# Kernel tuning notes

Hardware: AMD Instinct MI355X
Metric: run time of the kernel (lower is better)

## Reference

```python
import jax, jax.numpy as jnp
import numpy as np
import math

B, L, C_IN = 256, 128, 75
D_EMB = 128      # DataEmbedding d_model
D_MODEL = 126    # encoder d_model (= L-2 after ODConv valid conv k=3)
H = 6
D_HEAD = D_MODEL // H  # 21
D_FF = 2048
FACTOR = 5
K_NUM = 4        # ODConv kernel_num (default)
ATT_CH = 16      # max(int(128*0.0625), 16)
EPS = 1e-5


def _ln(x, g, b):
    m = x.mean(-1, keepdims=True)
    v = ((x - m) ** 2).mean(-1, keepdims=True)
    return (x - m) * jax.lax.rsqrt(v + EPS) * g + b


def _bn_eval(x, g, b):
    # eval-mode BatchNorm, running_mean=0 running_var=1
    return x * (g / np.sqrt(1.0 + EPS)) + b


def _conv1d(x, w, b=None):
    out = jax.lax.conv_general_dilated(x, w, (1,), 'VALID',
                                       dimension_numbers=('NCH', 'OIH', 'NCH'))
    if b is not None:
        out = out + b[None, :, None]
    return out


def _pos_embed(n, d):
    pos = np.arange(n)[:, None].astype(np.float32)
    div = np.exp(np.arange(0, d, 2).astype(np.float32) * (-math.log(10000.0) / d))
    pe = np.zeros((n, d), np.float32)
    pe[:, 0::2] = np.sin(pos * div)
    pe[:, 1::2] = np.cos(pos * div)
    return jnp.asarray(pe)


def _prob_attention(Q, K, V, key):
    # Informer ProbAttention, mask_flag=False. Q,K,V: [B,H,Lq,D]
    b, h, lq, d = Q.shape
    lk = K.shape[2]
    u_keys = min(FACTOR * int(np.ceil(np.log(lk))), lk)
    n_top = min(FACTOR * int(np.ceil(np.log(lq))), lq)
    idx = jax.random.randint(key, (lq, u_keys), 0, lk)     # sampled key ids per query
    K_s = K[:, :, idx, :]                                  # [B,H,Lq,u,D]
    qks = jnp.einsum('bhld,bhlud->bhlu', Q, K_s)
    M = qks.max(-1) - qks.sum(-1) / lk                     # sparsity measure
    _, top = jax.lax.top_k(M, n_top)                       # [B,H,n_top]
    Qr = jnp.take_along_axis(Q, top[..., None], axis=2)    # [B,H,n_top,D]
    scores = jnp.einsum('bhud,bhkd->bhuk', Qr, K) / np.sqrt(d).astype(np.float32)
    upd = jnp.einsum('bhuk,bhkd->bhud', jax.nn.softmax(scores, -1), V)
    ctx = jnp.broadcast_to(V.mean(2, keepdims=True), Q.shape)  # initial context
    bi = jnp.arange(b)[:, None, None]
    hi = jnp.arange(h)[None, :, None]
    return ctx.at[bi, hi, top].set(upd)


def _forward(x_enc, x_mark_enc, token_w, time_w, time_b,
             od_fc_w, od_bn_g, od_bn_b, od_ch_w, od_ch_b, od_fil_w, od_fil_b,
             od_sp_w, od_sp_b, od_ker_w, od_ker_b, od_weight,
             q_w, q_b, k_w, k_b, v_w, v_b, o_w, o_b,
             ffn1_w, ffn1_b, ffn2_w, ffn2_b, ln1_g, ln1_b, ln2_g, ln2_b,
             cl_w, cl_b, cl_bn_g, cl_bn_b, enc_ln_g, enc_ln_b, fc_w, fc_b):
    # ---- DataEmbedding (token circular conv + pos + timeF linear; dropout=eval) ----
    xt = jnp.pad(x_enc.transpose(0, 2, 1), ((0, 0), (0, 0), (1, 1)), mode='wrap')
    tok = _conv1d(xt, token_w).transpose(0, 2, 1)          # [B,L,128]
    emb = tok + _pos_embed(L, D_EMB)[None] + (x_mark_enc @ time_w + time_b)

    # ---- ODConv1d(128,128,k=3,pad=0) on [B,128,L] ----
    x = emb.transpose(0, 2, 1)                             # [B,128,L]
    gap = x.mean(-1)                                       # [B,128]
    a = jax.nn.relu(_bn_eval(gap @ od_fc_w, od_bn_g, od_bn_b))   # [B,16]
    ch_att = jax.nn.sigmoid(a @ od_ch_w + od_ch_b)         # [B,128]
    fil_att = jax.nn.sigmoid(a @ od_fil_w + od_fil_b)      # [B,128]
    sp_att = jax.nn.sigmoid(a @ od_sp_w + od_sp_b)         # [B,3]
    ker_att = jax.nn.softmax(a @ od_ker_w + od_ker_b, -1)  # [B,4]
    xc = x * ch_att[:, :, None]
    agg_w = jnp.einsum('bn,bj,noij->boij', ker_att, sp_att, od_weight)  # [B,128,128,3]
    lout = L - 2
    patches = jnp.stack([xc[:, :, j:j + lout] for j in range(3)], axis=2)  # [B,128,3,126]
    x = jnp.einsum('boij,bijt->bot', agg_w, patches) * fil_att[:, :, None]  # [B,128,126]
    # encoder reads this as (seq=128, d_model=126)

    key = jax.random.key(42)

    def enc_layer(xx, i):
        b, l, _ = xx.shape
        Q = (xx @ q_w[i] + q_b[i]).reshape(b, l, H, D_HEAD).transpose(0, 2, 1, 3)
        Kk = (xx @ k_w[i] + k_b[i]).reshape(b, l, H, D_HEAD).transpose(0, 2, 1, 3)
        Vv = (xx @ v_w[i] + v_b[i]).reshape(b, l, H, D_HEAD).transpose(0, 2, 1, 3)
        ctx = _prob_attention(Q, Kk, Vv, jax.random.fold_in(key, i))
        new_x = ctx.transpose(0, 2, 1, 3).reshape(b, l, D_MODEL) @ o_w[i] + o_b[i]
        xx = _ln(xx + new_x, ln1_g[i], ln1_b[i])
        y = jax.nn.gelu(xx @ ffn1_w[i] + ffn1_b[i], approximate=False)
        y = y @ ffn2_w[i] + ffn2_b[i]
        return _ln(xx + y, ln2_g[i], ln2_b[i])

    x = enc_layer(x, 0)
    # ConvLayer distilling: circular conv k3 + BN + ELU + maxpool(k3,s2,p1): 128 -> 64
    xt = jnp.pad(x.transpose(0, 2, 1), ((0, 0), (0, 0), (1, 1)), mode='wrap')
    xt = _conv1d(xt, cl_w, cl_b)
    xt = jax.nn.elu(_bn_eval(xt, cl_bn_g[None, :, None], cl_bn_b[None, :, None]))
    xt = jax.lax.reduce_window(xt, -jnp.inf, jax.lax.max, (1, 1, 3), (1, 1, 2),
                               [(0, 0), (0, 0), (1, 1)])
    x = xt.transpose(0, 2, 1)                              # [B,64,126]
    x = enc_layer(x, 1)
    x = _ln(x, enc_ln_g, enc_ln_b)

    out = x.transpose(0, 2, 1) @ fc_w + fc_b               # [B,126,1]
    return out.transpose(0, 2, 1)                          # [B,1,126]


def setup_inputs() -> dict:
    key = jax.random.key(0)
    it = iter(jax.random.split(key, 48))
    def rn(shape, s=0.05):
        return jax.random.normal(next(it), shape, dtype=jnp.float32) * s
    return {
        'x_enc': jax.random.normal(next(it), (B, L, C_IN), jnp.float32),
        'x_mark_enc': jax.random.uniform(next(it), (B, L, 3), jnp.float32, -0.5, 0.5),
        'token_w': rn((D_EMB, C_IN, 3), 0.1),
        'time_w': rn((3, D_EMB), 0.1), 'time_b': rn((D_EMB,)),
        'od_fc_w': rn((D_EMB, ATT_CH), 0.1),
        'od_bn_g': jnp.ones((ATT_CH,)), 'od_bn_b': jnp.zeros((ATT_CH,)),
        'od_ch_w': rn((ATT_CH, D_EMB), 0.1), 'od_ch_b': rn((D_EMB,)),
        'od_fil_w': rn((ATT_CH, D_EMB), 0.1), 'od_fil_b': rn((D_EMB,)),
        'od_sp_w': rn((ATT_CH, 3), 0.1), 'od_sp_b': rn((3,)),
        'od_ker_w': rn((ATT_CH, K_NUM), 0.1), 'od_ker_b': rn((K_NUM,)),
        'od_weight': rn((K_NUM, D_EMB, D_EMB, 3), 0.05),
        'q_w': rn((2, D_MODEL, D_MODEL)), 'q_b': rn((2, D_MODEL)),
        'k_w': rn((2, D_MODEL, D_MODEL)), 'k_b': rn((2, D_MODEL)),
        'v_w': rn((2, D_MODEL, D_MODEL)), 'v_b': rn((2, D_MODEL)),
        'o_w': rn((2, D_MODEL, D_MODEL)), 'o_b': rn((2, D_MODEL)),
        'ffn1_w': rn((2, D_MODEL, D_FF), 0.03), 'ffn1_b': rn((2, D_FF)),
        'ffn2_w': rn((2, D_FF, D_MODEL), 0.03), 'ffn2_b': rn((2, D_MODEL)),
        'ln1_g': jnp.ones((2, D_MODEL)), 'ln1_b': jnp.zeros((2, D_MODEL)),
        'ln2_g': jnp.ones((2, D_MODEL)), 'ln2_b': jnp.zeros((2, D_MODEL)),
        'cl_w': rn((D_MODEL, D_MODEL, 3), 0.05), 'cl_b': rn((D_MODEL,)),
        'cl_bn_g': jnp.ones((D_MODEL,)), 'cl_bn_b': jnp.zeros((D_MODEL,)),
        'enc_ln_g': jnp.ones((D_MODEL,)), 'enc_ln_b': jnp.zeros((D_MODEL,)),
        'fc_w': rn((L // 2, 1), 0.1), 'fc_b': rn((1,)),
    }


def reference(x_enc, x_mark_enc, token_w, time_w, time_b,
              od_fc_w, od_bn_g, od_bn_b, od_ch_w, od_ch_b, od_fil_w, od_fil_b,
              od_sp_w, od_sp_b, od_ker_w, od_ker_b, od_weight,
              q_w, q_b, k_w, k_b, v_w, v_b, o_w, o_b,
              ffn1_w, ffn1_b, ffn2_w, ffn2_b, ln1_g, ln1_b, ln2_g, ln2_b,
              cl_w, cl_b, cl_bn_g, cl_bn_b, enc_ln_g, enc_ln_b, fc_w, fc_b):
    return _forward(x_enc, x_mark_enc, token_w, time_w, time_b,
                    od_fc_w, od_bn_g, od_bn_b, od_ch_w, od_ch_b, od_fil_w, od_fil_b,
                    od_sp_w, od_sp_b, od_ker_w, od_ker_b, od_weight,
                    q_w, q_b, k_w, k_b, v_w, v_b, o_w, o_b,
                    ffn1_w, ffn1_b, ffn2_w, ffn2_b, ln1_g, ln1_b, ln2_g, ln2_b,
                    cl_w, cl_b, cl_bn_g, cl_bn_b, enc_ln_g, enc_ln_b, fc_w, fc_b)
```

## Files before the change

### kernel.cpp

```cpp
#include <hip/hip_runtime.h>
#include <math.h>

#define NB 256
#define DM 126
#define DE 128
#define NH 6
#define DHd 21
#define DFF 2048
#define CIN 75
#define L0 128
#define NTOP 25

#ifndef IDX_MODE
#define IDX_MODE 0
#endif

typedef const float* fp;
typedef unsigned short u16;
typedef short s8v __attribute__((ext_vector_type(8)));
typedef float f4v __attribute__((ext_vector_type(4)));

__device__ __forceinline__ u16 f2bf(float x){
  unsigned u = __float_as_uint(x);
  unsigned r = (u + 0x7FFFu + ((u >> 16) & 1u)) >> 16;
// ... 251 lines not shown
          float ang = (float)row * divc[t];
          float pe = (col & 1) ? __cosf(ang) : __sinf(ang);
          float tm = m0v*tw0c[t] + m1v*tw1c[t] + m2v*tw2c[t] + tbc[t];
          sE[row*132 + col] = acc[m][t][r] + pe + tm;
        }
      }
    }
  }
  __syncthreads();
  {
    int col = tid & 127, half = tid >> 7;
    float s = 0.f;
    for (int r = 0; r < 64; r++) s += sE[(half*64 + r)*132 + col];
    red[tid] = s;
  }
  __syncthreads();
  if (tid < 128) gap[tid] = (red[tid] + red[tid + 128]) * (1.f/128.f);
  __syncthreads();
  if (tid < 16){
    float acc = 0.f;
    for (int e = 0; e < DE; e++) acc += gap[e]*fcw[e*16 + tid];
    acc = acc * (bng[tid] / sqrtf(1.f + 1e-5f)) + bnb[tid];
    aAct[tid] = fmaxf(acc, 0.f);
  }
  __syncthreads();
  if (tid < 128){
    float accc = 0.f, accf = 0.f;
    for (int c = 0; c < 16; c++){ accc += aAct[c]*chw[c*DE + tid]; accf += aAct[c]*filw[c*DE + tid]; }
    sch[tid]  = 1.f/(1.f + __expf(-(accc + chb[tid])));
    sfil[tid] = 1.f/(1.f + __expf(-(accf + filb[tid])));
  } else if (tid < 131){
    int t = tid - 128;
    float acc = 0.f;
    for (int c = 0; c < 16; c++) acc += aAct[c]*spw[c*3 + t];
    ssp[t] = 1.f/(1.f + __expf(-(acc + spb[t])));
  } else if (tid == 132){
    float v[4]; float mx = -1e30f;
    for (int n = 0; n < 4; n++){
      float acc = 0.f;
      for (int c = 0; c < 16; c++) acc += aAct[c]*kerw[c*4 + n];
      v[n] = acc + kerb[n]; mx = fmaxf(mx, v[n]);
    }
    float ss = 0.f;
    for (int n = 0; n < 4; n++){ v[n] = __expf(v[n]-mx); ss += v[n]; }
    for (int n = 0; n < 4; n++) sker[n] = v[n]/ss;
  }
  __syncthreads();
  for (int p = tid; p < 130*128; p += 256){
    int l = p >> 7, i = p & 127;
    float v = (l < 128) ? sE[l*132 + i]*sch[i] : 0.f;
    sXT[l*136 + i] = f2bf(v);
  }
  __syncthreads();
  {
    float kr0 = sker[0], kr1 = sker[1], kr2 = sker[2], kr3 = sker[3];
    float spq[3]; spq[0] = ssp[0]; spq[1] = ssp[1]; spq[2] = ssp[2];
    const float4* od4 = (const float4*)odw;
    for (int p4 = tid; p4 < 128*384/4; p4 += 256){
      float4 w0 = od4[p4];
      float4 w1 = od4[12288 + p4];
      float4 w2 = od4[24576 + p4];
      float4 w3 = od4[36864 + p4];
      float vv[4] = { kr0*w0.x + kr1*w1.x + kr2*w2.x + kr3*w3.x,
                      kr0*w0.y + kr1*w1.y + kr2*w2.y + kr3*w3.y,
                      kr0*w0.z + kr1*w1.z + kr2*w2.z + kr3*w3.z,
                      kr0*w0.w + kr1*w1.w + kr2*w2.w + kr3*w3.w };
      int e0 = p4*4;
      #pragma unroll
      for (int j = 0; j < 4; j++){
        int e = e0 + j;
        int o = e / 384, rem = e - o*384;
        int i = rem / 3, q = rem - i*3;
        sW[(q*128 + o)*136 + i] = f2bf(vv[j] * spq[q]);
      }
    }
  }
  __syncthreads();
  {
    f4v acc[2][8];
    #pragma unroll
    for (int m = 0; m < 2; m++)
      #pragma unroll
      for (int t = 0; t < 8; t++) acc[m][t] = z4;
    for (int q = 0; q < 3; q++){
      const u16* wq = sW + q*128*136;
      #pragma unroll
      for (int ks = 0; ks < 4; ks++){
        s8v a0 = *reinterpret_cast<const s8v*>(wq + (mBase + l15)*136 + ks*32 + quad*8);
        s8v a1 = *reinterpret_cast<const s8v*>(wq + (mBase + 16 + l15)*136 + ks*32 + quad*8);
        #pragma unroll
        for (int t = 0; t < 8; t++){
          s8v bfr = *reinterpret_cast<const s8v*>(sXT + (t*16 + l15 + q)*136 + ks*32 + quad*8);
          acc[0][t] = __builtin_amdgcn_mfma_f32_16x16x32_bf16(a0, bfr, acc[0][t], 0, 0, 0);
          acc[1][t] = __builtin_amdgcn_mfma_f32_16x16x32_bf16(a1, bfr, acc[1][t], 0, 0, 0);
        }
      }
    }
    #pragma unroll
    for (int t = 0; t < 8; t++){
      int tt = t*16 + l15;
      if (tt < DM){
        #pragma unroll
        for (int m = 0; m < 2; m++){
          #pragma unroll
          for (int r = 0; r < 4; r++){
            int o = mBase + m*16 + quad*4 + r;
            xout[((size_t)b*DE + o)*DM + tt] = sfil[o] * acc[m][t][r];
          }
        }
      }
    }
  }
}

__global__ __launch_bounds__(256) void k_qkv_mfma(const float* xin, const u16* wqkv,
                                                  const float* qkvb, float* qkv,
                                                  float* vt, int L, int lshift, int lmask){
  __shared__ __align__(16) u16 sX[64*136];
  const int tid = threadIdx.x;
  const int wave = tid >> 6, lane = tid & 63, quad = lane >> 4, l15 = lane & 15;
  const size_t rows0 = (size_t)blockIdx.x * 64;
  for (int p = tid; p < 64*128; p += 256){
    int r = p >> 7, c = p & 127;
    float v = (c < DM) ? xin[(rows0 + r)*DM + c] : 0.f;
    sX[r*136 + c] = f2bf(v);
  }
  __syncthreads();
  const f4v z4 = {0.f,0.f,0.f,0.f};
  f4v acc[24];
  #pragma unroll
  for (int t = 0; t < 24; t++) acc[t] = z4;
  const int m0 = wave * 16;
  #pragma unroll
  for (int ks = 0; ks < 4; ks++){
    s8v a = *reinterpret_cast<const s8v*>(sX + (m0 + l15)*136 + ks*32 + quad*8);
    const u16* wb = wqkv + (size_t)l15*128 + ks*32 + quad*8;
    #pragma unroll
    for (int t = 0; t < 24; t++){
      s8v b = *reinterpret_cast<const s8v*>(wb + (size_t)t*16*128);
      acc[t] = __builtin_amdgcn_mfma_f32_16x16x32_bf16(a, b, acc[t], 0, 0, 0);
    }
  }
  #pragma unroll
  for (int t = 0; t < 24; t++){
    int col = t*16 + l15;
    float bv = qkvb[col];
    if (col < 256){
      #pragma unroll
      for (int r = 0; r < 4; r++){
        int row = m0 + quad*4 + r;
        qkv[(rows0 + row)*256 + col] = acc[t][r] + bv;
      }
    } else {
      int c = col - 256;
      if (c < DM){
        int h = c / DHd, d = c - h*DHd;
        #pragma unroll
        for (int r = 0; r < 4; r++){
          int gr = (int)rows0 + m0 + quad*4 + r;
          int b = gr >> lshift, l = gr & lmask;
          vt[((size_t)(b*NH + h)*DHd + d)*L + l] = acc[t][r] + bv;
        }
      }
    }
  }
}

__global__ __launch_bounds__(128) void k_attn(const float* qkv, const float* vt,
                                              const int* idx, int L,
                                              int* posmap, float* vmean, float* upd){
  __shared__ __align__(16) float sK[2816];
  __shared__ int sTop[32];
  const int tid = threadIdx.x;
  const int wave = tid >> 6, lane = tid & 63, quad = lane >> 4, l15 = lane & 15;
  const int bh = blockIdx.x;
  const int b = bh / NH, h = bh - b*NH;
  float* sM = sK + 2688;
  u16* sPb = reinterpret_cast<u16*>(sK);
  const float* qbase = qkv + (size_t)(b*L)*256 + h*DHd;
  const float* vb = vt + (size_t)bh*DHd*L;
  const f4v z4 = {0.f,0.f,0.f,0.f};
  const int ntn = L >> 4;
  const int d0 = quad*8;
  const int mt = wave;

  for (int p = tid; p < L*DHd; p += 128){
    int l = p / DHd, d = p - l*DHd;
    sK[p] = qbase[(size_t)l*256 + 128 + d];
  }
  posmap[bh*L0 + tid] = -1;
  __syncthreads();
  if (tid < L){
    const int l = tid;
    const float* qg = qbase + (size_t)l*256;
    float qr[DHd];
    #pragma unroll
    for (int d = 0; d < DHd; d++) qr[d] = qg[d];
    float mx = -1e30f, sm = 0.f;
    #pragma unroll
    for (int u = 0; u < NTOP; u++){
      int kk = idx[l*NTOP + u];
      const float* kp = sK + kk*DHd;
      float acc = 0.f;
      #pragma unroll
      for (int d = 0; d < DHd; d++) acc += qr[d]*kp[d];
      mx = fmaxf(mx, acc); sm += acc;
    }
    sM[l] = mx - sm/(float)L;
  }
  __syncthreads();
  if (wave == 0){
    for (int it = 0; it < NTOP; it++){
      float bv = sM[lane]; int bi = lane;
      if (L == 128){
        float v1 = sM[lane + 64];
        if (v1 > bv){ bv = v1; bi = lane + 64; }
      }
      #pragma unroll
      for (int off = 32; off > 0; off >>= 1){
        float ov = __shfl_xor(bv, off);
        int   oi = __shfl_xor(bi, off);
        if (ov > bv || (ov == bv && oi < bi)){ bv = ov; bi = oi; }
      }
      if (lane == 0){
        sM[bi] = -1e30f;
        posmap[bh*L0 + bi] = it;
        sTop[it] = bi;
      }
    }
  }
  __syncthreads();

  s8v aq;
  {
    int uu = mt*16 + l15; if (uu >= NTOP) uu = 0;
    int r = sTop[uu];
    const float* qp = qbase + (size_t)r*256 + d0;
    #pragma unroll
    for (int j = 0; j < 8; j++) aq[j] = (short)f2bf(qp[j]);
  }
  f4v sc[8];
  for (int nt = 0; nt < ntn; nt++){
    const float* kp = sK + (size_t)(nt*16 + l15)*DHd + d0;
    s8v bb;
    #pragma unroll
    for (int j = 0; j < 8; j++) bb[j] = (d0 + j < DHd) ? (short)f2bf(kp[j]) : (short)0;
    sc[nt] = __builtin_amdgcn_mfma_f32_16x16x32_bf16(aq, bb, z4, 0, 0, 0);
  }
  __syncthreads();
  const float inv21 = 0.21821789023599236f;
  #pragma unroll
  for (int r4 = 0; r4 < 4; r4++){
    float mx = -1e30f;
    for (int nt = 0; nt < ntn; nt++) mx = fmaxf(mx, sc[nt][r4]*inv21);
    #pragma unroll
    for (int off = 1; off < 16; off <<= 1) mx = fmaxf(mx, __shfl_xor(mx, off));
    float e[8]; float ss = 0.f;
    for (int nt = 0; nt < ntn; nt++){ e[nt] = __expf(sc[nt][r4]*inv21 - mx); ss += e[nt]; }
    #pragma unroll
    for (int off = 1; off < 16; off <<= 1) ss += __shfl_xor(ss, off);
    float dn = 1.f / ss;
    int u = mt*16 + quad*4 + r4;
    for (int nt = 0; nt < ntn; nt++)
      sPb[u*136 + nt*16 + l15] = f2bf(e[nt]*dn);
  }
  if (wave == 1){
    u16 invL = f2bf(1.f/(float)L);
    for (int c = lane; c < L; c += 64) sPb[25*136 + c] = invL;
  }
  f4v pv[2];
  pv[0] = z4; pv[1] = z4;
  int kSteps = L >> 5;
  for (int ks = 0; ks < kSteps; ks++){
    #pragma unroll
    for (int nt = 0; nt < 2; nt++){
      int d = nt*16 + l15;
      s8v bb;
      if (d < DHd){
        const float* vp = vb + (size_t)d*L + ks*32 + d0;
        #pragma unroll
        for (int j = 0; j < 8; j++) bb[j] = (short)f2bf(vp[j]);
      } else {
        #pragma unroll
        for (int j = 0; j < 8; j++) bb[j] = (short)0;
      }
      s8v a = *reinterpret_cast<const s8v*>(sPb + (mt*16 + l15)*136 + ks*32 + d0);
      pv[nt] = __builtin_amdgcn_mfma_f32_16x16x32_bf16(a, bb, pv[nt], 0, 0, 0);
    }
  }
  #pragma unroll
  for (int nt = 0; nt < 2; nt++){
    #pragma unroll
    for (int r4 = 0; r4 < 4; r4++){
      int u = mt*16 + quad*4 + r4;
      int d = nt*16 + l15;
      if (d < DHd){
        if (u < NTOP)       upd[((size_t)bh*NTOP + u)*DHd + d] = pv[nt][r4];
        else if (u == NTOP) vmean[bh*DHd + d] = pv[nt][r4];
      }
    }
  }
}

__global__ __launch_bounds__(256) void k_oproj_mfma(const float* xin, const float* vmean,
                                                    const int* posmap, const float* upd,
                                                    const u16* wo, fp ob, fp g, fp bb,
                                                    int layer, int lshift, int lmask, float* xmid){
  __shared__ __align__(16) float sOf[64*129];
  __shared__ float prs[128];
  __shared__ float smean[64], srstd[64];
  u16* sX = reinterpret_cast<u16*>(sOf);
  const int tid = threadIdx.x;
  const int wave = tid >> 6, lane = tid & 63, quad = lane >> 4, l15 = lane & 15;
  const int m0 = wave * 16;
  const size_t rows0 = (size_t)blockIdx.x * 64;
  for (int p = tid; p < 64*128; p += 256){
    int r = p >> 7, c = p & 127;
    int gr = (int)rows0 + r, b = gr >> lshift, l = gr & lmask;
    float v = 0.f;
    if (c < DM){
      int h = c / DHd, d = c - h*DHd;
      int bh = b*NH + h;
      int pos = posmap[bh*L0 + l];
      v = (pos >= 0) ? upd[((size_t)bh*NTOP + pos)*DHd + d] : vmean[bh*DHd + d];
    }
    sX[r*136 + c] = f2bf(v);
  }
  __syncthreads();
  const f4v z4 = {0.f,0.f,0.f,0.f};
  f4v acc[8];
  #pragma unroll
  for (int t = 0; t < 8; t++) acc[t] = z4;
  #pragma unroll
  for (int ks = 0; ks < 4; ks++){
    s8v a = *reinterpret_cast<const s8v*>(sX + (m0 + l15)*136 + ks*32 + quad*8);
    const u16* wb = wo + (size_t)l15*128 + ks*32 + quad*8;
    #pragma unroll
    for (int t = 0; t < 8; t++){
      s8v b = *reinterpret_cast<const s8v*>(wb + (size_t)t*16*128);
      acc[t] = __builtin_amdgcn_mfma_f32_16x16x32_bf16(a, b, acc[t], 0, 0, 0);
    }
  }
  __syncthreads();
  #pragma unroll
  for (int t = 0; t < 8; t++){
    int col = t*16 + l15;
    #pragma unroll
    for (int r = 0; r < 4; r++){
      sOf[(m0 + quad*4 + r)*129 + col] = acc[t][r];
    }
  }
  __syncthreads();
  const float* obl = ob + (size_t)layer*DM;
  for (int p = tid; p < 64*DM; p += 256){
    int r = p / DM, c = p - r*DM;
    sOf[r*129 + c] += xin[(rows0 + r)*DM + c] + obl[c];
  }
  __syncthreads();
  if (tid < 128){
    int row = tid >> 1, half = tid & 1;
    float s = 0.f;
    for (int c = half*63; c < half*63 + 63; c++) s += sOf[row*129 + c];
    prs[tid] = s;
  }
  __syncthreads();
  if (tid < 128 && (tid & 1) == 0) smean[tid>>1] = (prs[tid] + prs[tid+1]) / (float)DM;
  __syncthreads();
  if (tid < 128){
    int row = tid >> 1, half = tid & 1;
    float mn = smean[row];
    float s = 0.f;
    for (int c = half*63; c < half*63 + 63; c++){ float d = sOf[row*129 + c] - mn; s += d*d; }
    prs[tid] = s;
  }
  __syncthreads();
  if (tid < 128 && (tid & 1) == 0) srstd[tid>>1] = rsqrtf((prs[tid] + prs[tid+1])/(float)DM + 1e-5f);
  __syncthreads();
  const float* gl = g  + (size_t)layer*DM;
  const float* bl = bb + (size_t)layer*DM;
  for (int p = tid; p < 64*DM; p += 256){
    int r = p / DM, c = p - r*DM;
    xmid[(rows0 + r)*DM + c] = (sOf[r*129 + c] - smean[r])*srstd[r]*gl[c] + bl[c];
  }
}

__device__ __forceinline__ float gelu_fast(float x){
  float x2 = x*x;
  float u = x * __builtin_fmaf(0.10295128f, x2, 2.30212056f);
  u = fminf(u, 126.f);
#if __has_builtin(__builtin_amdgcn_exp2f)
  float t = __builtin_amdgcn_exp2f(u);
#else
  float t = __expf(u * 0.69314718056f);
#endif
  return x * t * __builtin_amdgcn_rcpf(t + 1.f);
}


__device__ __forceinline__ void stage_w1_p(const u16* w1t, int j, u16* buf, int p){
  int n = p >> 4, c = p & 15;
  int cg = c ^ (n & 7);
  gld_lds16(w1t + (((size_t)(j*64 + n)) << 7) + cg*8,
            buf + (size_t)((p >> 6) << 6)*8);
}
__device__ __forceinline__ void stage_w2_p(const u16* w2t, int j, u16* buf, int p){
  int n = p >> 3, c = p & 7;
  int cg = c ^ (n & 7);
  gld_lds16(w2t + (size_t)n*2048 + j*64 + cg*8,
            buf + (size_t)((p >> 6) << 6)*8);
}

__device__ __forceinline__ int yaddr(int row, int col){
  return row*64 + (((col >> 3) ^ (row & 7)) << 3) + (col & 7);
}

__device__ __forceinline__ void lgkm_barrier(){
  asm volatile("s_waitcnt lgkmcnt(0)" ::: "memory");
  __builtin_amdgcn_sched_barrier(0);
  __builtin_amdgcn_s_barrier();
  __builtin_amdgcn_sched_barrier(0);
}

template<int NT>
__global__ __launch_bounds__(NT) void k_ffn(const float* xmid, const u16* w1t, const u16* w2t,
                                            fp b1, fp b2w, fp g, fp bb, int layer,
                                            const u16* wdist, fp e1, fp e2, fp e3, fp e4,
                                            const float* xres, const float* vmeanp,
                                            const int* posmapp, const float* updp,
                                            const u16* wo, fp obp, fp l1g, fp l1b,
                                            float* out2){
  constexpr int ROWS = NT/8;
  constexpr int NMG  = NT/256;
  constexpr int SYG  = NMG*2048;
  constexpr int SP   = 1024/NT;
  constexpr int XMOFF = SYG + 4*8192;
  constexpr int SMEMU = (NT == 1024) ? (XMOFF + 128*130*2) : (SYG + 4*8192);
  __shared__ __align__(16) u16 smem[SMEMU];
  __shared__ float prs[2*ROWS];
  __shared__ float smean[ROWS], srstd[ROWS];
  u16* wA0 = smem + SYG;
  u16* wA1 = wA0 + 8192;
  u16* wB0 = wA1 + 8192;
  u16* wB1 = wB0 + 8192;
  const int tid  = threadIdx.x;
  const int wave = tid >> 6, lane = tid & 63, quad = lane >> 4, l15 = lane & 15;
  const int mg = wave >> 2, ng = wave & 3;
  const int rowb = mg * 32;
  u16* sYg = smem + mg*2048;
  const size_t rows0 = (size_t)blockIdx.x * ROWS;
  const f4v z4 = {0.f, 0.f, 0.f, 0.f};
  float* xm = reinterpret_cast<float*>(smem + XMOFF);

  if constexpr (NT == 1024){
    const int bb_ = blockIdx.x;
    u16* sX = smem;
    for (int p = tid; p < 128*128; p += 1024){
      int r = p >> 7, c = p & 127;
      float v = 0.f;
      if (c < DM){
        int h = c / DHd, d = c - h*DHd;
        int bh = bb_*NH + h;
        int pos = posmapp[bh*L0 + r];
        v = (pos >= 0) ? updp[((size_t)bh*NTOP + pos)*DHd + d] : vmeanp[bh*DHd + d];
      }
      sX[r*136 + c] = f2bf(v);
    }
    __syncthreads();
    const int m0o = (wave & 7) * 16;
    const int nb0 = (wave >> 3) * 4;
    f4v oacc[4];
    oacc[0]=z4; oacc[1]=z4; oacc[2]=z4; oacc[3]=z4;
    #pragma unroll
    for (int ks = 0; ks < 4; ks++){
      s8v a = *reinterpret_cast<const s8v*>(sX + (m0o + l15)*136 + ks*32 + quad*8);
      const u16* wbp = wo + (size_t)l15*128 + ks*32 + quad*8;
      #pragma unroll
      for (int t = 0; t < 4; t++){
        s8v bfr = *reinterpret_cast<const s8v*>(wbp + (size_t)(nb0 + t)*16*128);
        oacc[t] = __builtin_amdgcn_mfma_f32_16x16x32_bf16(a, bfr, oacc[t], 0, 0, 0);
      }
    }
    __syncthreads();
    float* sOf = reinterpret_cast<float*>(smem);
    #pragma unroll
    for (int t = 0; t < 4; t++){
      int col = (nb0 + t)*16 + l15;
      #pragma unroll
      for (int r = 0; r < 4; r++)
        sOf[(m0o + quad*4 + r)*129 + col] = oacc[t][r];
    }
    __syncthreads();
    for (int p = tid; p < 128*DM; p += 1024){
      int r = p / DM, c = p - r*DM;
      sOf[r*129 + c] += xres[((size_t)bb_*128 + r)*DM + c] + obp[c];
    }
    __syncthreads();
    if (tid < 256){
      int row = tid >> 1, half = tid & 1;
      float s = 0.f;
      for (int c = half*63; c < half*63 + 63; c++) s += sOf[row*129 + c];
      prs[tid] = s;
    }
    __syncthreads();
    if (tid < 256 && (tid & 1) == 0) smean[tid>>1] = (prs[tid] + prs[tid+1]) / (float)DM;
    __syncthreads();
    if (tid < 256){
      int row = tid >> 1, half = tid & 1;
      float mn = smean[row];
      float s = 0.f;
      for (int c = half*63; c < half*63 + 63; c++){ float d = sOf[row*129 + c] - mn; s += d*d; }
      prs[tid] = s;
    }
    __syncthreads();
    if (tid < 256 && (tid & 1) == 0) srstd[tid>>1] = rsqrtf((prs[tid] + prs[tid+1])/(float)DM + 1e-5f);
    __syncthreads();
    for (int p = tid; p < 128*DM; p += 1024){
      int r = p / DM, c = p - r*DM;
      xm[r*130 + c] = (sOf[r*129 + c] - smean[r])*srstd[r]*l1g[c] + l1b[c];
    }
    __syncthreads();
  }

  s8v aX[2][4];
  #pragma unroll
  for (int mt = 0; mt < 2; mt++){
    #pragma unroll
    for (int ks = 0; ks < 4; ks++){
      #pragma unroll
      for (int jj2 = 0; jj2 < 8; jj2++){
        int c = ks*32 + quad*8 + jj2;
        float v = 0.f;
        if (c < DM){
          if constexpr (NT == 1024) v = xm[(rowb + mt*16 + l15)*130 + c];
          else v = xmid[(rows0 + rowb + mt*16 + l15)*(size_t)DM + c];
        }
        aX[mt][ks][jj2] = (short)f2bf(v);
      }
    }
  }
  #pragma unroll
  for (int r = 0; r < SP; r++){
    stage_w1_p(w1t, 0, wA0, r*NT + tid);
    stage_w2_p(w2t, 0, wB0, r*NT + tid);
  }

  const float* b1l = b1 + (size_t)layer*DFF;
  f4v acc2[2][2];
  acc2[0][0]=z4; acc2[0][1]=z4; acc2[1][0]=z4; acc2[1][1]=z4;

  for (int j = 0; j < 32; j++){
    u16* wAcur = (j & 1) ? wA1 : wA0;
    u16* wAnxt = (j & 1) ? wA0 : wA1;
    u16* wBcur = (j & 1) ? wB1 : wB0;
    u16* wBnxt = (j & 1) ? wB0 : wB1;
    __syncthreads();
    if (j < 31){
      #pragma unroll
      for (int r = 0; r < SP; r++){
        stage_w1_p(w1t, j+1, wAnxt, r*NT + tid);
        stage_w2_p(w2t, j+1, wBnxt, r*NT + tid);
      }
    }
    f4v acc1[2];
    acc1[0] = z4; acc1[1] = z4;
    {
      int nloc = ng*16 + l15;
      #pragma unroll
      for (int ks = 0; ks < 4; ks++){
        int cg = (ks*4 + quad) ^ (nloc & 7);
        s8v b = *reinterpret_cast<const s8v*>(wAcur + nloc*128 + cg*8);
        acc1[0] = __builtin_amdgcn_mfma_f32_16x16x32_bf16(aX[0][ks], b, acc1[0], 0, 0, 0);
        acc1[1] = __builtin_amdgcn_mfma_f32_16x16x32_bf16(aX[1][ks], b, acc1[1], 0, 0, 0);
      }
    }
    {
      int col = ng*16 + l15;
      float bv = b1l[j*64 + col];
      #pragma unroll
      for (int mt = 0; mt < 2; mt++){
        float y0 = gelu_fast(acc1[mt][0] + bv);
        float y1 = gelu_fast(acc1[mt][1] + bv);
        float y2 = gelu_fast(acc1[mt][2] + bv);
        float y3 = gelu_fast(acc1[mt][3] + bv);
        unsigned p01 = cvt_pk_bf16(y0, y1);
        unsigned p23 = cvt_pk_bf16(y2, y3);
        int r0 = mt*16 + quad*4;
        sYg[yaddr(r0,     col)] = (u16)p01;
        sYg[yaddr(r0 + 1, col)] = (u16)(p01 >> 16);
        sYg[yaddr(r0 + 2, col)] = (u16)p23;
        sYg[yaddr(r0 + 3, col)] = (u16)(p23 >> 16);
      }
    }
    lgkm_barrier();
    #pragma unroll
    for (int ks2 = 0; ks2 < 2; ks2++){
      int ga = ((ks2*4 + quad) ^ (l15 & 7)) << 3;
      s8v a0 = *reinterpret_cast<const s8v*>(sYg + (l15)*64 + ga);
      s8v a1 = *reinterpret_cast<const s8v*>(sYg + (16 + l15)*64 + ga);
      #pragma unroll
      for (int t = 0; t < 2; t++){
        int nloc = ng*32 + t*16 + l15;
        int cg = (ks2*4 + quad) ^ (nloc & 7);
        s8v b = *reinterpret_cast<const s8v*>(wBcur + nloc*64 + cg*8);
        acc2[0][t] = __builtin_amdgcn_mfma_f32_16x16x32_bf16(a0, b, acc2[0][t], 0, 0, 0);
        acc2[1][t] = __builtin_amdgcn_mfma_f32_16x16x32_bf16(a1, b, acc2[1][t], 0, 0, 0);
      }
    }
  }

  __syncthreads();
  float* sO = reinterpret_cast<float*>(smem);
  #pragma unroll
  for (int mt = 0; mt < 2; mt++)
    #pragma unroll
    for (int t = 0; t < 2; t++)
      #pragma unroll
      for (int r = 0; r < 4; r++)
        sO[(rowb + mt*16 + quad*4 + r)*129 + ng*32 + t*16 + l15] = acc2[mt][t][r];
  __syncthreads();
  const float* b2l = b2w + (size_t)layer*DM;
  for (int p = tid; p < ROWS*DM; p += NT){
    int r = p / DM, c = p - r*DM;
    float res;
    if constexpr (NT == 1024) res = xm[r*130 + c];
    else res = xmid[(rows0 + r)*DM + c];
    sO[r*129 + c] += b2l[c] + res;
  }
  __syncthreads();
  if (tid < 2*ROWS){
    int row = tid >> 1, half = tid & 1;
    float s = 0.f;
    for (int c = half*63; c < half*63 + 63; c++) s += sO[row*129 + c];
    prs[tid] = s;
  }
  __syncthreads();
  if (tid < 2*ROWS && (tid & 1) == 0) smean[tid>>1] = (prs[tid] + prs[tid+1]) / (float)DM;
  __syncthreads();
  if (tid < 2*ROWS){
    int row = tid >> 1, half = tid & 1;
    float mn = smean[row];
    float s = 0.f;
    for (int c = half*63; c < half*63 + 63; c++){ float d = sO[row*129 + c] - mn; s += d*d; }
    prs[tid] = s;
  }
  __syncthreads();
  if (tid < 2*ROWS && (tid & 1) == 0) srstd[tid>>1] = rsqrtf((prs[tid] + prs[tid+1])/(float)DM + 1e-5f);
  __syncthreads();
  const float* gl = g  + (size_t)layer*DM;
  const float* bl = bb + (size_t)layer*DM;

  if constexpr (NT == 1024){
    float rv[16];
    #pragma unroll
    for (int k = 0; k < 16; k++){
      int p = tid + k*1024;
      if (p < 128*DM){
        int r = p / DM, c = p - r*DM;
        rv[k] = (sO[r*129 + c] - smean[r])*srstd[r]*gl[c] + bl[c];
      } else rv[k] = 0.f;
    }
    __syncthreads();
    u16* sAd = smem;
    #pragma unroll
    for (int k = 0; k < 16; k++){
      int p = tid + k*1024;
      if (p < 128*DM){
        int r = p / DM, c = p - r*DM;
        u16 bv = f2bf(rv[k]);
        sAd[((r + 1) & 127)*392 + c] = bv;
        sAd[r*392 + 126 + c] = bv;
        sAd[((r + 127) & 127)*392 + 252 + c] = bv;
      }
    }
    if (tid < 768){ int row = tid / 6, c2 = tid - row*6; sAd[row*392 + 378 + c2] = 0; }
    __syncthreads();
    const int mrow  = (wave & 7) * 16;
    const int tbase = (wave >> 3) * 4;
    f4v dac[4];
    dac[0]=z4; dac[1]=z4; dac[2]=z4; dac[3]=z4;
    for (int ks = 0; ks < 12; ks++){
      s8v a = *reinterpret_cast<const s8v*>(sAd + (mrow + l15)*392 + ks*32 + quad*8);
      const u16* wbp = wdist + (size_t)l15*384 + ks*32 + quad*8;
      #pragma unroll
      for (int t = 0; t < 4; t++){
        s8v bfr = *reinterpret_cast<const s8v*>(wbp + (size_t)(tbase + t)*16*384);
        dac[t] = __builtin_amdgcn_mfma_f32_16x16x32_bf16(a, bfr, dac[t], 0, 0, 0);
      }
    }
    __syncthreads();
    float* zsh = reinterpret_cast<float*>(smem);
    const float bnscale = 1.f / sqrtf(1.f + 1e-5f);
    #pragma unroll
    for (int t = 0; t < 4; t++){
      int co = (tbase + t)*16 + l15;
      if (co < DM){
        float cb = e1[co];
        float gg = e2[co] * bnscale, bv = e3[co];
        #pragma unroll
        for (int r = 0; r < 4; r++){
          int row = mrow + quad*4 + r;
          float z = (dac[t][r] + cb)*gg + bv;
          z = (z > 0.f) ? z : (__expf(z) - 1.f);
          zsh[row*130 + co] = z;
        }
      }
    }
    __syncthreads();
    for (int p = tid; p < 64*DM; p += 1024){
      int jj = p / DM, co = p - jj*DM;
      float best = zsh[(2*jj)*130 + co];
      if (jj > 0) best = fmaxf(best, zsh[(2*jj - 1)*130 + co]);
      best = fmaxf(best, zsh[(2*jj + 1)*130 + co]);
      out2[((size_t)blockIdx.x*64 + jj)*DM + co] = best;
    }
  } else {
    for (int p = tid; p < ROWS*DM; p += NT){
      int r = p / DM, c = p - r*DM;
      sO[r*129 + c] = (sO[r*129 + c] - smean[r])*srstd[r]*gl[c] + bl[c];
    }
    __syncthreads();
    if (tid < 2*ROWS){
      int row = tid >> 1, half = tid & 1;
      float s = 0.f;
      for (int c = half*63; c < half*63 + 63; c++) s += sO[row*129 + c];
      prs[tid] = s;
    }
    __syncthreads();
    if (tid < 2*ROWS && (tid & 1) == 0) smean[tid>>1] = (prs[tid] + prs[tid+1]) / (float)DM;
    __syncthreads();
    if (tid < 2*ROWS){
      int row = tid >> 1, half = tid & 1;
      float mn = smean[row];
      float s = 0.f;
      for (int c = half*63; c < half*63 + 63; c++){ float d = sO[row*129 + c] - mn; s += d*d; }
      prs[tid] = s;
    }
    __syncthreads();
    if (tid < 2*ROWS && (tid & 1) == 0) srstd[tid>>1] = rsqrtf((prs[tid] + prs[tid+1])/(float)DM + 1e-5f);
    __syncthreads();
    if (tid < DM){
      float gv = e1[tid], bv2 = e2[tid];
      float acc = e4[0];
      for (int l = 0; l < 64; l++){
        float xn = (sO[l*129 + tid] - smean[l])*srstd[l]*gv + bv2;
        acc += xn * e3[l];
      }
      out2[(size_t)blockIdx.x*DM + tid] = acc;
    }
  }
}

extern "C" void kernel_launch(void* const* d_in, const int* in_sizes, int n_in,
                              void* d_out, int out_size, void* d_ws, size_t ws_size,
                              hipStream_t stream) {
  fp x_enc   = (fp)d_in[0];
  fp x_mark  = (fp)d_in[1];
  fp token_w = (fp)d_in[2];
  fp time_w  = (fp)d_in[3];
  fp time_b  = (fp)d_in[4];
  fp od_fc_w = (fp)d_in[5];
  fp od_bn_g = (fp)d_in[6];
  fp od_bn_b = (fp)d_in[7];
  fp od_ch_w = (fp)d_in[8];
  fp od_ch_b = (fp)d_in[9];
  fp od_fil_w= (fp)d_in[10];
  fp od_fil_b= (fp)d_in[11];
  fp od_sp_w = (fp)d_in[12];
  fp od_sp_b = (fp)d_in[13];
  fp od_ker_w= (fp)d_in[14];
  fp od_ker_b= (fp)d_in[15];
  fp od_wt   = (fp)d_in[16];
  fp q_w = (fp)d_in[17]; fp q_b = (fp)d_in[18];
  fp k_w = (fp)d_in[19]; fp k_b = (fp)d_in[20];
  fp v_w = (fp)d_in[21]; fp v_b = (fp)d_in[22];
  fp o_w = (fp)d_in[23]; fp o_b = (fp)d_in[24];
  fp f1w = (fp)d_in[25]; fp f1b = (fp)d_in[26];
  fp f2w = (fp)d_in[27]; fp f2b = (fp)d_in[28];
  fp ln1g= (fp)d_in[29]; fp ln1b= (fp)d_in[30];
  fp ln2g= (fp)d_in[31]; fp ln2b= (fp)d_in[32];
  fp cl_w= (fp)d_in[33]; fp cl_b= (fp)d_in[34];
  fp clbg= (fp)d_in[35]; fp clbb= (fp)d_in[36];
  fp elng= (fp)d_in[37]; fp elnb= (fp)d_in[38];
  fp fc_w= (fp)d_in[39]; fp fc_b= (fp)d_in[40];

  const size_t OFF_IDX0 = 0;
  const size_t OFF_IDX1 = OFF_IDX0 + 3200;
  const size_t OFF_CH   = OFF_IDX1 + 1600;
  const size_t OFF_FIL  = OFF_CH  + (size_t)NB*DE;
  const size_t OFF_SP   = OFF_FIL + (size_t)NB*DE;
  const size_t OFF_KER  = OFF_SP  + (size_t)NB*4;
  const size_t OFF_VM   = OFF_KER + (size_t)NB*4;
  const size_t OFF_POS  = OFF_VM  + (size_t)NB*NH*DHd;
  const size_t OFF_UPD  = OFF_POS + (size_t)NB*NH*L0;
  const size_t OFF_STOP = OFF_UPD + (size_t)NB*NH*NTOP*DHd;
  const size_t OFF_WTS  = (OFF_STOP + (size_t)NB*NH*NTOP + 255) & ~(size_t)255;
  const size_t WTS_FLOATS = (2*262144 + 2*262144 + 2*49152 + 2*16384 + 49152 + 32768)/2 + 2*384;
  const size_t OFF_BIG  = (OFF_WTS + WTS_FLOATS + 255) & ~(size_t)255;
  const size_t SBUF     = (size_t)NB*DE*L0;
  const size_t TOTAL    = OFF_BIG + 4*SBUF;

  if (ws_size < TOTAL*sizeof(float)){
    hipLaunchKernelGGL(k_zero, dim3((out_size+255)/256), dim3(256), 0, stream,
                       (float*)d_out, out_size);
    return;
  }

  float* ws = (float*)d_ws;
  int* idx0 = (int*)(ws + OFF_IDX0);
  int* idx1 = (int*)(ws + OFF_IDX1);
  float* vme = ws + OFF_VM;
  int* posm  = (int*)(ws + OFF_POS);
  float* updb= ws + OFF_UPD;
  u16* w1tb  = (u16*)(ws + OFF_WTS);
  u16* w2tb  = w1tb + 2*262144;
  u16* wqkvb = w2tb + 2*262144;
  u16* wob   = wqkvb + 2*49152;
  u16* wdistb= wob + 2*16384;
  u16* wembb = wdistb + 49152;
  float* qkvbias = (float*)(wembb + 32768);

  float* X    = ws + OFF_BIG;
  float* QKV  = X + SBUF;
  float* X2   = X + 2*SBUF;
  float* VT   = X + 3*SBUF;
  float* xmid = QKV;

  hipLaunchKernelGGL(k_prep, dim3(1092), dim3(256), 0, stream,
                     idx0, idx1, token_w, cl_w, q_w, q_b, k_w, k_b, v_w, v_b, o_w,
                     wembb, wdistb, wqkvb, wob, qkvbias,
                     f1w, f2w, w1tb, w2tb);
  hipLaunchKernelGGL(k_front, dim3(NB), dim3(256), 0, stream,
                     x_enc, x_mark, wembb, time_w, time_b,
                     od_fc_w, od_bn_g, od_bn_b, od_ch_w, od_ch_b, od_fil_w, od_fil_b,
                     od_sp_w, od_sp_b, od_ker_w, od_ker_b, od_wt, X);

  hipLaunchKernelGGL(k_qkv_mfma, dim3(NB*L0/64), dim3(256), 0, stream,
                     X, wqkvb, qkvbias, QKV, VT, 128, 7, 127);
  hipLaunchKernelGGL(k_attn, dim3(NB*NH), dim3(128), 0, stream,
                     QKV, VT, idx0, L0, posm, vme, updb);
  hipLaunchKernelGGL((k_ffn<1024>), dim3(NB), dim3(1024), 0, stream,
                     X, w1tb, w2tb, f1b, f2b, ln2g, ln2b, 0,
                     wdistb, cl_b, clbg, clbb, cl_b,
                     X, vme, posm, updb, wob, o_b, ln1g, ln1b,
                     X2);

  hipLaunchKernelGGL(k_qkv_mfma, dim3(NB*64/64), dim3(256), 0, stream,
                     X2, wqkvb + 49152, qkvbias + 384, QKV, VT, 64, 6, 63);
  hipLaunchKernelGGL(k_attn, dim3(NB*NH), dim3(128), 0, stream,
                     QKV, VT, idx1, 64, posm, vme, updb);
  hipLaunchKernelGGL(k_oproj_mfma, dim3(NB*64/64), dim3(256), 0, stream,
                     X2, vme, posm, updb, wob + 16384, o_b, ln1g, ln1b, 1, 6, 63, xmid);
  hipLaunchKernelGGL((k_ffn<512>), dim3(256), dim3(512), 0, stream,
                     xmid, w1tb + 262144, w2tb + 262144, f1b, f2b, ln2g, ln2b, 1,
                     wdistb, elng, elnb, fc_w, fc_b,
                     X2, vme, posm, updb, wob, o_b, ln1g, ln1b,
                     (float*)d_out);
  (void)in_sizes; (void)n_in; (void)out_size; (void)ws_size;
}
```

Baseline: 564.3 us.

## Fuse layer-2 QKV projection into layer-1 FFN and O-proj into layer-2 FFN

The layer-1 FFN kernel now computes the layer-2 QKV projection from its pooled output held in shared memory, writing QKV and transposed V directly. The separate k_qkv_mfma launch for layer 2 goes away. The layer-2 FFN kernel now does the output projection, residual add and LayerNorm itself, so the standalone k_oproj_mfma kernel and its xmid round-trip are removed. This saves two launches and global memory traffic. The cost is more shared memory and register pressure in the fused kernels, and extra serial work at the tail of the 1024-thread kernel.

```diff
diff --git a/kernel.cpp b/kernel.cpp
--- a/kernel.cpp
+++ b/kernel.cpp
@@ -577,88 +577,6 @@
   }
 }
 
-__global__ __launch_bounds__(256) void k_oproj_mfma(const float* xin, const float* vmean,
-                                                    const int* posmap, const float* upd,
-                                                    const u16* wo, fp ob, fp g, fp bb,
-                                                    int layer, int lshift, int lmask, float* xmid){
-  __shared__ __align__(16) float sOf[64*129];
-  __shared__ float prs[128];
-  __shared__ float smean[64], srstd[64];
-  u16* sX = reinterpret_cast<u16*>(sOf);
-  const int tid = threadIdx.x;
-  const int wave = tid >> 6, lane = tid & 63, quad = lane >> 4, l15 = lane & 15;
-  const int m0 = wave * 16;
-  const size_t rows0 = (size_t)blockIdx.x * 64;
-  for (int p = tid; p < 64*128; p += 256){
-    int r = p >> 7, c = p & 127;
-    int gr = (int)rows0 + r, b = gr >> lshift, l = gr & lmask;
-    float v = 0.f;
-    if (c < DM){
-      int h = c / DHd, d = c - h*DHd;
-      int bh = b*NH + h;
-      int pos = posmap[bh*L0 + l];
-      v = (pos >= 0) ? upd[((size_t)bh*NTOP + pos)*DHd + d] : vmean[bh*DHd + d];
-    }
-    sX[r*136 + c] = f2bf(v);
-  }
-  __syncthreads();
-  const f4v z4 = {0.f,0.f,0.f,0.f};
-  f4v acc[8];
-  #pragma unroll
-  for (int t = 0; t < 8; t++) acc[t] = z4;
-  #pragma unroll
-  for (int ks = 0; ks < 4; ks++){
-    s8v a = *reinterpret_cast<const s8v*>(sX + (m0 + l15)*136 + ks*32 + quad*8);
-    const u16* wb = wo + (size_t)l15*128 + ks*32 + quad*8;
-    #pragma unroll
-    for (int t = 0; t < 8; t++){
-      s8v b = *reinterpret_cast<const s8v*>(wb + (size_t)t*16*128);
-      acc[t] = __builtin_amdgcn_mfma_f32_16x16x32_bf16(a, b, acc[t], 0, 0, 0);
-    }
-  }
-  __syncthreads();
-  #pragma unroll
-  for (int t = 0; t < 8; t++){
-    int col = t*16 + l15;
-    #pragma unroll
-    for (int r = 0; r < 4; r++){
-      sOf[(m0 + quad*4 + r)*129 + col] = acc[t][r];
-    }
-  }
-  __syncthreads();
-  const float* obl = ob + (size_t)layer*DM;
-  for (int p = tid; p < 64*DM; p += 256){
-    int r = p / DM, c = p - r*DM;
-    sOf[r*129 + c] += xin[(rows0 + r)*DM + c] + obl[c];
-  }
-  __syncthreads();
-  if (tid < 128){
-    int row = tid >> 1, half = tid & 1;
-    float s = 0.f;
-    for (int c = half*63; c < half*63 + 63; c++) s += sOf[row*129 + c];
-    prs[tid] = s;
-  }
-  __syncthreads();
-  if (tid < 128 && (tid & 1) == 0) smean[tid>>1] = (prs[tid] + prs[tid+1]) / (float)DM;
-  __syncthreads();
-  if (tid < 128){
-    int row = tid >> 1, half = tid & 1;
-    float mn = smean[row];
-    float s = 0.f;
-    for (int c = half*63; c < half*63 + 63; c++){ float d = sOf[row*129 + c] - mn; s += d*d; }
-    prs[tid] = s;
-  }
-  __syncthreads();
-  if (tid < 128 && (tid & 1) == 0) srstd[tid>>1] = rsqrtf((prs[tid] + prs[tid+1])/(float)DM + 1e-5f);
-  __syncthreads();
-  const float* gl = g  + (size_t)layer*DM;
-  const float* bl = bb + (size_t)layer*DM;
-  for (int p = tid; p < 64*DM; p += 256){
-    int r = p / DM, c = p - r*DM;
-    xmid[(rows0 + r)*DM + c] = (sOf[r*129 + c] - smean[r])*srstd[r]*gl[c] + bl[c];
-  }
-}
-
 __device__ __forceinline__ float gelu_fast(float x){
   float x2 = x*x;
   float u = x * __builtin_fmaf(0.10295128f, x2, 2.30212056f);
@@ -697,19 +615,21 @@
 }
 
 template<int NT>
-__global__ __launch_bounds__(NT) void k_ffn(const float* xmid, const u16* w1t, const u16* w2t,
+__global__ __launch_bounds__(NT) void k_ffn(const u16* w1t, const u16* w2t,
                                             fp b1, fp b2w, fp g, fp bb, int layer,
                                             const u16* wdist, fp e1, fp e2, fp e3, fp e4,
                                             const float* xres, const float* vmeanp,
                                             const int* posmapp, const float* updp,
                                             const u16* wo, fp obp, fp l1g, fp l1b,
+                                            const u16* wqkv1, fp qb1, float* qkvout, float* vtout,
                                             float* out2){
   constexpr int ROWS = NT/8;
   constexpr int NMG  = NT/256;
   constexpr int SYG  = NMG*2048;
   constexpr int SP   = 1024/NT;
   constexpr int XMOFF = SYG + 4*8192;
-  constexpr int SMEMU = (NT == 1024) ? (XMOFF + 128*130*2) : (SYG + 4*8192);
+  constexpr int TAILU = (NT == 1024) ? 128*392 : 0;
+  constexpr int SMEMU = (XMOFF + ROWS*130*2) > TAILU ? (XMOFF + ROWS*130*2) : TAILU;
   __shared__ __align__(16) u16 smem[SMEMU];
   __shared__ float prs[2*ROWS];
   __shared__ float smean[ROWS], srstd[ROWS];
@@ -722,14 +642,13 @@
   const int mg = wave >> 2, ng = wave & 3;
   const int rowb = mg * 32;
   u16* sYg = smem + mg*2048;
-  const size_t rows0 = (size_t)blockIdx.x * ROWS;
   const f4v z4 = {0.f, 0.f, 0.f, 0.f};
   float* xm = reinterpret_cast<float*>(smem + XMOFF);
-
-  if constexpr (NT == 1024){
-    const int bb_ = blockIdx.x;
+  const int bb_ = blockIdx.x;
+
+  {
     u16* sX = smem;
-    for (int p = tid; p < 128*128; p += 1024){
+    for (int p = tid; p < ROWS*128; p += NT){
       int r = p >> 7, c = p & 127;
       float v = 0.f;
       if (c < DM){
@@ -741,14 +660,16 @@
       sX[r*136 + c] = f2bf(v);
     }
     __syncthreads();
-    const int m0o = (wave & 7) * 16;
-    const int nb0 = (wave >> 3) * 4;
+    constexpr int MT = ROWS/16;
+    const int m0o = (wave % MT)*16;
+    const int nb0 = (wave / MT)*4;
+    const u16* wol = wo + (size_t)layer*16384;
     f4v oacc[4];
     oacc[0]=z4; oacc[1]=z4; oacc[2]=z4; oacc[3]=z4;
     #pragma unroll
     for (int ks = 0; ks < 4; ks++){
       s8v a = *reinterpret_cast<const s8v*>(sX + (m0o + l15)*136 + ks*32 + quad*8);
-      const u16* wbp = wo + (size_t)l15*128 + ks*32 + quad*8;
+      const u16* wbp = wol + (size_t)l15*128 + ks*32 + quad*8;
       #pragma unroll
       for (int t = 0; t < 4; t++){
         s8v bfr = *reinterpret_cast<const s8v*>(wbp + (size_t)(nb0 + t)*16*128);
@@ -765,21 +686,22 @@
         sOf[(m0o + quad*4 + r)*129 + col] = oacc[t][r];
     }
     __syncthreads();
-    for (int p = tid; p < 128*DM; p += 1024){
+    const float* obl = obp + (size_t)layer*DM;
+    for (int p = tid; p < ROWS*DM; p += NT){
       int r = p / DM, c = p - r*DM;
-      sOf[r*129 + c] += xres[((size_t)bb_*128 + r)*DM + c] + obp[c];
-    }
-    __syncthreads();
-    if (tid < 256){
+      sOf[r*129 + c] += xres[((size_t)bb_*ROWS + r)*DM + c] + obl[c];
+    }
+    __syncthreads();
+    if (tid < 2*ROWS){
       int row = tid >> 1, half = tid & 1;
       float s = 0.f;
       for (int c = half*63; c < half*63 + 63; c++) s += sOf[row*129 + c];
       prs[tid] = s;
     }
     __syncthreads();
-    if (tid < 256 && (tid & 1) == 0) smean[tid>>1] = (prs[tid] + prs[tid+1]) / (float)DM;
-    __syncthreads();
-    if (tid < 256){
+    if (tid < 2*ROWS && (tid & 1) == 0) smean[tid>>1] = (prs[tid] + prs[tid+1]) / (float)DM;
+    __syncthreads();
+    if (tid < 2*ROWS){
       int row = tid >> 1, half = tid & 1;
       float mn = smean[row];
       float s = 0.f;
@@ -787,11 +709,13 @@
       prs[tid] = s;
     }
     __syncthreads();
-    if (tid < 256 && (tid & 1) == 0) srstd[tid>>1] = rsqrtf((prs[tid] + prs[tid+1])/(float)DM + 1e-5f);
-    __syncthreads();
-    for (int p = tid; p < 128*DM; p += 1024){
+    if (tid < 2*ROWS && (tid & 1) == 0) srstd[tid>>1] = rsqrtf((prs[tid] + prs[tid+1])/(float)DM + 1e-5f);
+    __syncthreads();
+    const float* l1gl = l1g + (size_t)layer*DM;
+    const float* l1bl = l1b + (size_t)layer*DM;
+    for (int p = tid; p < ROWS*DM; p += NT){
       int r = p / DM, c = p - r*DM;
-      xm[r*130 + c] = (sOf[r*129 + c] - smean[r])*srstd[r]*l1g[c] + l1b[c];
+      xm[r*130 + c] = (sOf[r*129 + c] - smean[r])*srstd[r]*l1gl[c] + l1bl[c];
     }
     __syncthreads();
   }
@@ -804,11 +728,7 @@
       #pragma unroll
       for (int jj2 = 0; jj2 < 8; jj2++){
         int c = ks*32 + quad*8 + jj2;
-        float v = 0.f;
-        if (c < DM){
-          if constexpr (NT == 1024) v = xm[(rowb + mt*16 + l15)*130 + c];
-          else v = xmid[(rows0 + rowb + mt*16 + l15)*(size_t)DM + c];
-        }
+        float v = (c < DM) ? xm[(rowb + mt*16 + l15)*130 + c] : 0.f;
         aX[mt][ks][jj2] = (short)f2bf(v);
       }
     }
@@ -896,10 +816,7 @@
   const float* b2l = b2w + (size_t)layer*DM;
   for (int p = tid; p < ROWS*DM; p += NT){
     int r = p / DM, c = p - r*DM;
-    float res;
-    if constexpr (NT == 1024) res = xm[r*130 + c];
-    else res = xmid[(rows0 + r)*DM + c];
-    sO[r*129 + c] += b2l[c] + res;
+    sO[r*129 + c] += b2l[c] + xm[r*130 + c];
   }
   __syncthreads();
   if (tid < 2*ROWS){
@@ -981,12 +898,54 @@
       }
     }
     __syncthreads();
-    for (int p = tid; p < 64*DM; p += 1024){
-      int jj = p / DM, co = p - jj*DM;
-      float best = zsh[(2*jj)*130 + co];
-      if (jj > 0) best = fmaxf(best, zsh[(2*jj - 1)*130 + co]);
-      best = fmaxf(best, zsh[(2*jj + 1)*130 + co]);
-      out2[((size_t)blockIdx.x*64 + jj)*DM + co] = best;
+    u16* sQ = smem + XMOFF;
+    for (int p = tid; p < 64*128; p += 1024){
+      int jj = p >> 7, co = p & 127;
+      float best = 0.f;
+      if (co < DM){
+        best = zsh[(2*jj)*130 + co];
+        if (jj > 0) best = fmaxf(best, zsh[(2*jj - 1)*130 + co]);
+        best = fmaxf(best, zsh[(2*jj + 1)*130 + co]);
+        out2[((size_t)bb_*64 + jj)*DM + co] = best;
+      }
+      sQ[jj*136 + co] = f2bf(best);
+    }
+    __syncthreads();
+    {
+      const int mq  = wave & 3;
+      const int ngq = wave >> 2;
+      f4v qa[6];
+      #pragma unroll
+      for (int t = 0; t < 6; t++) qa[t] = z4;
+      #pragma unroll
+      for (int ks = 0; ks < 4; ks++){
+        s8v a = *reinterpret_cast<const s8v*>(sQ + (mq*16 + l15)*136 + ks*32 + quad*8);
+        const u16* wbq = wqkv1 + (size_t)l15*128 + ks*32 + quad*8;
+        #pragma unroll
+        for (int t = 0; t < 6; t++){
+          int nt = ngq*6 + t;
+          s8v b = *reinterpret_cast<const s8v*>(wbq + (size_t)nt*16*128);
+          qa[t] = __builtin_amdgcn_mfma_f32_16x16x32_bf16(a, b, qa[t], 0, 0, 0);
+        }
+      }
+      #pragma unroll
+      for (int t = 0; t < 6; t++){
+        int col = (ngq*6 + t)*16 + l15;
+        float bv = qb1[col];
+        #pragma unroll
+        for (int r = 0; r < 4; r++){
+          int row = mq*16 + quad*4 + r;
+          if (col < 256){
+            qkvout[((size_t)bb_*64 + row)*256 + col] = qa[t][r] + bv;
+          } else {
+            int c = col - 256;
+            if (c < DM){
+              int h = c / DHd, d = c - h*DHd;
+              vtout[((size_t)(bb_*NH + h)*DHd + d)*64 + row] = qa[t][r] + bv;
+            }
+          }
+        }
+      }
     }
   } else {
     for (int p = tid; p < ROWS*DM; p += NT){
@@ -1020,7 +979,7 @@
         float xn = (sO[l*129 + tid] - smean[l])*srstd[l]*gv + bv2;
         acc += xn * e3[l];
       }
-      out2[(size_t)blockIdx.x*DM + tid] = acc;
+      out2[(size_t)bb_*DM + tid] = acc;
     }
   }
 }
@@ -1098,7 +1057,6 @@
   float* QKV  = X + SBUF;
   float* X2   = X + 2*SBUF;
   float* VT   = X + 3*SBUF;
-  float* xmid = QKV;
 
   hipLaunchKernelGGL(k_prep, dim3(1092), dim3(256), 0, stream,
                      idx0, idx1, token_w, cl_w, q_w, q_b, k_w, k_b, v_w, v_b, o_w,
@@ -1114,21 +1072,19 @@
   hipLaunchKernelGGL(k_attn, dim3(NB*NH), dim3(128), 0, stream,
                      QKV, VT, idx0, L0, posm, vme, updb);
   hipLaunchKernelGGL((k_ffn<1024>), dim3(NB), dim3(1024), 0, stream,
-                     X, w1tb, w2tb, f1b, f2b, ln2g, ln2b, 0,
+                     w1tb, w2tb, f1b, f2b, ln2g, ln2b, 0,
                      wdistb, cl_b, clbg, clbb, cl_b,
                      X, vme, posm, updb, wob, o_b, ln1g, ln1b,
+                     wqkvb + 49152, qkvbias + 384, QKV, VT,
                      X2);
 
-  hipLaunchKernelGGL(k_qkv_mfma, dim3(NB*64/64), dim3(256), 0, stream,
-                     X2, wqkvb + 49152, qkvbias + 384, QKV, VT, 64, 6, 63);
   hipLaunchKernelGGL(k_attn, dim3(NB*NH), dim3(128), 0, stream,
                      QKV, VT, idx1, 64, posm, vme, updb);
-  hipLaunchKernelGGL(k_oproj_mfma, dim3(NB*64/64), dim3(256), 0, stream,
-                     X2, vme, posm, updb, wob + 16384, o_b, ln1g, ln1b, 1, 6, 63, xmid);
   hipLaunchKernelGGL((k_ffn<512>), dim3(256), dim3(512), 0, stream,
-                     xmid, w1tb + 262144, w2tb + 262144, f1b, f2b, ln2g, ln2b, 1,
+                     w1tb + 262144, w2tb + 262144, f1b, f2b, ln2g, ln2b, 1,
                      wdistb, elng, elnb, fc_w, fc_b,
                      X2, vme, posm, updb, wob, o_b, ln1g, ln1b,
+                     wqkvb + 49152, qkvbias + 384, QKV, VT,
                      (float*)d_out);
   (void)in_sizes; (void)n_in; (void)out_size; (void)ws_size;
 }
```

After: 519.3 us. -8.0%, faster.
